# Performance work log

Hardware: AMD Instinct MI355X
Metric: run time of the kernel (lower is better)

The kernel has to match this reference:

```python
import jax, jax.numpy as jnp
import numpy as np

N = 100000
E = 2000000
F = 64          # in_features == out_features (required by attention * h_j)
BETA = 0.5
NEG_SLOPE = 0.01  # torch F.leaky_relu default


def setup_inputs() -> dict:
    key = jax.random.key(0)
    k1, k2, k3, k4, k5, k6 = jax.random.split(key, 6)
    h = jax.random.normal(k1, (N, F), dtype=jnp.float32)
    adj = jax.random.randint(k2, (2, E), 0, N, dtype=jnp.int64)
    amount = jax.random.uniform(k3, (E,), dtype=jnp.float32)
    count = jax.random.uniform(k4, (E,), dtype=jnp.float32)
    fc_w = jax.random.normal(k5, (F, 2 * F), dtype=jnp.float32) * (1.0 / np.sqrt(2 * F))
    fc_b = jax.random.normal(k6, (F,), dtype=jnp.float32) * 0.01
    return {"h": h, "adj": adj, "amount": amount, "count": count,
            "fc_w": fc_w, "fc_b": fc_b}


def _minmax_norm(x):
    lo, hi = x.min(), x.max()
    return (x - lo) / (hi - lo + 1e-8)


def reference(h, adj, amount, count, fc_w, fc_b):
    # per-edge weight from normalized amount/count
    edge_weight = BETA * _minmax_norm(amount) + (1.0 - BETA) * _minmax_norm(count)  # [E]

    src, dst = adj[0], adj[1]
    h_i = h[src]                     # [E, F]
    h_j = h[dst]                     # [E, F]
    h_cat = jnp.concatenate([h_i, h_j], axis=1)  # [E, 2F]

    score = jnp.einsum('ef,of->eo', h_cat, fc_w) + fc_b  # [E, F_out]
    score = jnp.where(score >= 0, score, NEG_SLOPE * score)  # leaky_relu
    score = score * edge_weight[:, None]

    # softmax over ALL edges (dim 0), per feature, as in the original
    attention = jax.nn.softmax(score, axis=0)  # [E, F]

    agg = jnp.zeros_like(h).at[src].add(attention * h_j)  # scatter-add -> [N, F]
    return agg
```

## Files before the change

kernel.cpp:

```cpp
#include <hip/hip_runtime.h>
#include <hip/hip_fp16.h>
#include <math.h>

#define FDIM   64
#define NB     16
#define BSHIFT 7
#define BMASK  127
#define EPTA   16
#define CHUNKA (EPTA * 256)
#define SCH    1024
#define DMASK  0xFFFFF

__global__ __launch_bounds__(256) void count_mm_k(const int* __restrict__ src,
                                                  const float* __restrict__ amount,
                                                  const float* __restrict__ count,
                                                  int* __restrict__ mat,
                                                  float4* __restrict__ partial,
                                                  double* __restrict__ colsum,
                                                  int E, int nblkA, int nbkt) {
  __shared__ int lhist[1024];
  __shared__ float4 lred[4];
  for (int k = threadIdx.x; k < nbkt; k += 256) lhist[k] = 0;
  if (blockIdx.x == 0 && threadIdx.x < 64) colsum[threadIdx.x] = 0.0;
  __syncthreads();
  float amin = 3.4e38f, amax = -3.4e38f, cmin = 3.4e38f, cmax = -3.4e38f;
  int e0 = blockIdx.x * CHUNKA + threadIdx.x * EPTA;
  if (e0 + EPTA <= E) {
    #pragma unroll
    for (int q = 0; q < EPTA; q += 4) {
      int4   s4 = *(const int4*)(src + e0 + q);
      float4 a4 = *(const float4*)(amount + e0 + q);
      float4 c4 = *(const float4*)(count + e0 + q);
      atomicAdd(&lhist[s4.x >> BSHIFT], 1);
      atomicAdd(&lhist[s4.y >> BSHIFT], 1);
      atomicAdd(&lhist[s4.z >> BSHIFT], 1);
      atomicAdd(&lhist[s4.w >> BSHIFT], 1);
      amin = fminf(amin, fminf(fminf(a4.x, a4.y), fminf(a4.z, a4.w)));
      amax = fmaxf(amax, fmaxf(fmaxf(a4.x, a4.y), fmaxf(a4.z, a4.w)));
      cmin = fminf(cmin, fminf(fminf(c4.x, c4.y), fminf(c4.z, c4.w)));
      cmax = fmaxf(cmax, fmaxf(fmaxf(c4.x, c4.y), fmaxf(c4.z, c4.w)));
    }
  } else {
    for (int e = e0; e < E; e++) {
      atomicAdd(&lhist[src[e] >> BSHIFT], 1);
      float a = amount[e], c = count[e];
      amin = fminf(amin, a); amax = fmaxf(amax, a);
      cmin = fminf(cmin, c); cmax = fmaxf(cmax, c);
    }
  }
  #pragma unroll
  for (int off = 32; off; off >>= 1) {
    amin = fminf(amin, __shfl_down(amin, off));
    amax = fmaxf(amax, __shfl_down(amax, off));
    cmin = fminf(cmin, __shfl_down(cmin, off));
    cmax = fmaxf(cmax, __shfl_down(cmax, off));
  }
  if ((threadIdx.x & 63) == 0) lred[threadIdx.x >> 6] = make_float4(amin, amax, cmin, cmax);
  __syncthreads();
  for (int k = threadIdx.x; k < nbkt; k += 256)
    mat[(size_t)k * nblkA + blockIdx.x] = lhist[k];
  if (threadIdx.x == 0) {
    float4 r = lred[0];
    #pragma unroll
    for (int w = 1; w < 4; w++) {
      r.x = fminf(r.x, lred[w].x); r.y = fmaxf(r.y, lred[w].y);
      r.z = fminf(r.z, lred[w].z); r.w = fmaxf(r.w, lred[w].w);
    }
    partial[blockIdx.x] = r;
  }
}

__global__ __launch_bounds__(256) void minmax2_k(const float4* __restrict__ partial,
                                                 float* __restrict__ mmf, int nb) {
  float amin = 3.4e38f, amax = -3.4e38f, cmin = 3.4e38f, cmax = -3.4e38f;
  for (int i = threadIdx.x; i < nb; i += 256) {
    float4 p = partial[i];
    amin = fminf(amin, p.x); amax = fmaxf(amax, p.y);
    cmin = fminf(cmin, p.z); cmax = fmaxf(cmax, p.w);
  }
  #pragma unroll
  for (int off = 32; off; off >>= 1) {
    amin = fminf(amin, __shfl_down(amin, off));
    amax = fmaxf(amax, __shfl_down(amax, off));
    cmin = fminf(cmin, __shfl_down(cmin, off));
    cmax = fmaxf(cmax, __shfl_down(cmax, off));
  }
  __shared__ float4 lds[4];
  if ((threadIdx.x & 63) == 0) lds[threadIdx.x >> 6] = make_float4(amin, amax, cmin, cmax);
  __syncthreads();
  if (threadIdx.x == 0) {
    float4 r = lds[0];
    #pragma unroll
    for (int w = 1; w < 4; w++) {
      r.x = fminf(r.x, lds[w].x); r.y = fmaxf(r.y, lds[w].y);
      r.z = fminf(r.z, lds[w].z); r.w = fmaxf(r.w, lds[w].w);
    }
    mmf[0] = r.x; mmf[1] = r.y; mmf[2] = r.z; mmf[3] = r.w;
  }
}

__global__ __launch_bounds__(256) void scan1_k(const int* __restrict__ v,
                                               int* __restrict__ bsum, int M) {
  __shared__ int lds[256];
  int t = threadIdx.x, b = blockIdx.x;
  int s = 0;
  for (int i = b * SCH + t; i < min((b + 1) * SCH, M); i += 256) s += v[i];
  lds[t] = s; __syncthreads();
  for (int off = 128; off; off >>= 1) {
    if (t < off) lds[t] += lds[t + off];
    __syncthreads();
  }
  if (t == 0) bsum[b] = lds[0];
}

__global__ __launch_bounds__(256) void scan2_k(const int* __restrict__ bsum,
                                               int* __restrict__ bexcl, int nchunk) {
  __shared__ int lds[256];
  int t = threadIdx.x;
  int running = 0;
  for (int c0 = 0; c0 < nchunk; c0 += 256) {
    int x = (c0 + t < nchunk) ? bsum[c0 + t] : 0;
    lds[t] = x; __syncthreads();
    for (int off = 1; off < 256; off <<= 1) {
      int v = (t >= off) ? lds[t - off] : 0;
      __syncthreads();
      lds[t] += v; __syncthreads();
    }
    if (c0 + t < nchunk) bexcl[c0 + t] = running + lds[t] - x;
    running += lds[255];
    __syncthreads();
  }
}

__global__ __launch_bounds__(256) void scan3_k(const int* __restrict__ v,
                                               const int* __restrict__ bexcl,
                                               int* __restrict__ smat, int M) {
  __shared__ int lds[256];
  int t = threadIdx.x, b = blockIdx.x;
  int running = bexcl[b];
  for (int tile = 0; tile < SCH; tile += 256) {
    int i = b * SCH + tile + t;
    int x = (i < M) ? v[i] : 0;
    lds[t] = x; __syncthreads();
    for (int off = 1; off < 256; off <<= 1) {
      int vv = (t >= off) ? lds[t - off] : 0;
      __syncthreads();
      lds[t] += vv; __syncthreads();
    }
    if (i < M) smat[i] = running + lds[t] - x;
    running += lds[255];
    __syncthreads();
  }
}

__global__ __launch_bounds__(256) void scatter_k(const int* __restrict__ src,
                                                 const int* __restrict__ dst,
                                                 const float* __restrict__ amount,
                                                 const float* __restrict__ count,
                                                 const float* __restrict__ mmf,
                                                 const int* __restrict__ smat,
                                                 int2* __restrict__ payload,
                                                 int E, int nblkA, int nbkt) {
  __shared__ int cntb[1024];
  __shared__ int baseb[1024];
  __shared__ int sbase[1024];
  __shared__ int tmp[256];
  __shared__ int2 lpay[CHUNKA];
  __shared__ int lgpos[CHUNKA];
  const int t = threadIdx.x, blk = blockIdx.x;
  for (int k = t; k < nbkt; k += 256) {
    cntb[k] = 0;
    sbase[k] = smat[(size_t)k * nblkA + blk];
  }
  __syncthreads();
  const float amin = mmf[0], amax = mmf[1], cmin = mmf[2], cmax = mmf[3];
  const float ascale = 0.5f / (amax - amin + 1e-8f);
  const float cscale = 0.5f / (cmax - cmin + 1e-8f);
  int e0 = blk * CHUNKA + t * EPTA;
  const bool full = (e0 + EPTA <= E);
  int4   S[4]; int4 D[4]; float4 A[4]; float4 C[4];
  if (full) {
    #pragma unroll
    for (int q = 0; q < 4; q++) {
      S[q] = *(const int4*)(src + e0 + 4 * q);
      D[q] = *(const int4*)(dst + e0 + 4 * q);
      A[q] = *(const float4*)(amount + e0 + 4 * q);
      C[q] = *(const float4*)(count + e0 + 4 * q);
      atomicAdd(&cntb[S[q].x >> BSHIFT], 1);
      atomicAdd(&cntb[S[q].y >> BSHIFT], 1);
      atomicAdd(&cntb[S[q].z >> BSHIFT], 1);
      atomicAdd(&cntb[S[q].w >> BSHIFT], 1);
    }
  } else {
    for (int e = e0; e < E; e++) atomicAdd(&cntb[src[e] >> BSHIFT], 1);
  }
  __syncthreads();
  int running = 0;
  for (int c0 = 0; c0 < nbkt; c0 += 256) {
    int x = (c0 + t < nbkt) ? cntb[c0 + t] : 0;
    tmp[t] = x; __syncthreads();
    for (int off = 1; off < 256; off <<= 1) {
      int v = (t >= off) ? tmp[t - off] : 0;
      __syncthreads();
      tmp[t] += v; __syncthreads();
    }
    if (c0 + t < nbkt) baseb[c0 + t] = running + tmp[t] - x;
    running += tmp[255];
    __syncthreads();
  }
  for (int k = t; k < nbkt; k += 256) cntb[k] = baseb[k];
  __syncthreads();
  auto ins = [&](int s, int d, float a, float c) {
    int b = s >> BSHIFT;
    float ew = (a - amin) * ascale + (c - cmin) * cscale;
    int pos = atomicAdd(&cntb[b], 1);
    lpay[pos] = make_int2(d | ((s & BMASK) << 20), __float_as_int(ew));
    lgpos[pos] = sbase[b] + (pos - baseb[b]);
  };
  if (full) {
    #pragma unroll
    for (int q = 0; q < 4; q++) {
      ins(S[q].x, D[q].x, A[q].x, C[q].x);
      ins(S[q].y, D[q].y, A[q].y, C[q].y);
      ins(S[q].z, D[q].z, A[q].z, C[q].z);
      ins(S[q].w, D[q].w, A[q].w, C[q].w);
    }
  } else {
    for (int e = e0; e < E; e++) ins(src[e], dst[e], amount[e], count[e]);
  }
  __syncthreads();
  const int ned = min(CHUNKA, E - blk * CHUNKA);
  for (int i = t; i < ned; i += 256) payload[lgpos[i]] = lpay[i];
}

__global__ __launch_bounds__(256) void binB_k(const int2* __restrict__ payload,
                                              const int* __restrict__ smat,
                                              int* __restrict__ hist,
                                              int* __restrict__ offsets,
                                              int2* __restrict__ edge_s,
                                              int E, int nblkA, int nbkt, int N) {
  __shared__ int fcnt[128];
  __shared__ int fs[128];
  __shared__ int fcur[128];
  const int b = blockIdx.x;
  const int t = threadIdx.x;
  const int base = smat[(size_t)b * nblkA];
  const int end  = (b + 1 < nbkt) ? smat[(size_t)(b + 1) * nblkA] : E;
  if (t < 128) fcnt[t] = 0;
  __syncthreads();
  for (int i = base + t; i < end; i += 256)
    atomicAdd(&fcnt[payload[i].x >> 20], 1);
  __syncthreads();
  if (t < 128) fs[t] = fcnt[t];
  __syncthreads();
  for (int off = 1; off < 128; off <<= 1) {
    int v = 0;
    if (t < 128 && t >= off) v = fs[t - off];
    __syncthreads();
    if (t < 128) fs[t] += v;
    __syncthreads();
  }
  if (t < 128) {
    int excl = fs[t] - fcnt[t];
    fcur[t] = base + excl;
    int node = (b << BSHIFT) + t;
    if (node < N) { hist[node] = fcnt[t]; offsets[node] = base + excl; }
  }
  __syncthreads();
  for (int i = base + t; i < end; i += 256) {
    int2 v = payload[i];
    int pos = atomicAdd(&fcur[v.x >> 20], 1);
    edge_s[pos] = make_int2(v.x & DMASK, v.y);
  }
}

__global__ __launch_bounds__(128) void pre_gemm(const float* __restrict__ h,
                                                const float* __restrict__ fc_w,
                                                const float* __restrict__ fc_b,
                                                float* __restrict__ G1,
                                                __half2* __restrict__ P, int N) {
  __shared__ float hs[NB * FDIM];
  const int t = threadIdx.x;
  const int o = t & 63, half = t >> 6;
  float w[FDIM];
  const float* wrow = fc_w + o * 128 + half * 64;
  #pragma unroll
  for (int f = 0; f < FDIM; f += 4) {
    float4 v = *(const float4*)(wrow + f);
    w[f] = v.x; w[f + 1] = v.y; w[f + 2] = v.z; w[f + 3] = v.w;
  }
  const float bias = (half == 0) ? fc_b[o] : 0.0f;
  const int n0 = blockIdx.x * NB;
  const int nrows = min(NB, N - n0);
  for (int i = t; i < nrows * FDIM; i += 128) hs[i] = h[(size_t)n0 * FDIM + i];
  __syncthreads();
  for (int n = 0; n < nrows; n++) {
    float acc = bias;
    #pragma unroll
    for (int f = 0; f < FDIM; f += 4) {
      float4 hv = *(const float4*)(&hs[n * FDIM + f]);
      acc += hv.x * w[f] + hv.y * w[f + 1] + hv.z * w[f + 2] + hv.w * w[f + 3];
    }
    if (half == 0) {
      G1[(size_t)(n0 + n) * FDIM + o] = acc;
    } else {
      P[(size_t)(n0 + n) * FDIM + o] =
          __halves2half2(__float2half(acc), __float2half(hs[n * FDIM + o]));
    }
  }
}

__device__ __forceinline__ float2 unpack_h2(unsigned u) {
  __half2 v = *(__half2*)&u;
  return make_float2(__low2float(v), __high2float(v));
}

__global__ __launch_bounds__(256) void fused_k(const int* __restrict__ offsets,
                                               const int* __restrict__ hist,
                                               const int2* __restrict__ edge_s,
                                               const float* __restrict__ G1,
                                               const unsigned* __restrict__ P,
                                               double* __restrict__ colsum,
                                               float* __restrict__ out, int N) {
  const int lane = threadIdx.x & 63;
  const int wid = blockIdx.x * 4 + (threadIdx.x >> 6);
  const int nw = gridDim.x * 4;
  float csum = 0.0f;
  int n = wid;
  int start = 0, cnt = 0;
  int2 p0 = make_int2(0, 0);
  float g1 = 0.0f;
  if (n < N) {
    start = offsets[n]; cnt = hist[n];
    g1 = G1[(size_t)n * FDIM + lane];
    if (lane < cnt) p0 = edge_s[start + lane];
  }
  while (n < N) {
    int nn = n + nw;
    int startN = 0, cntN = 0; float g1N = 0.0f;
    if (nn < N) {
      startN = offsets[nn]; cntN = hist[nn];
      g1N = G1[(size_t)nn * FDIM + lane];
    }
    float acc = 0.0f;
    for (int j0 = 0; j0 < cnt; j0 += 64) {
      int m = min(64, cnt - j0);
      int2 p;
      if (j0 == 0) p = p0;
      else { p = make_int2(0, 0); if (lane < m) p = edge_s[start + j0 + lane]; }
      for (int j = 0; j < m; j += 8) {
        int rem = m - j;
        int dd[8]; float ee[8], wm[8]; unsigned uu[8];
        #pragma unroll
        for (int k = 0; k < 8; k++) {
          dd[k] = __builtin_amdgcn_readlane(p.x, j + k);
          ee[k] = __int_as_float(__builtin_amdgcn_readlane(p.y, j + k));
          wm[k] = (k < rem) ? 1.0f : 0.0f;
        }
        #pragma unroll
        for (int k = 0; k < 8; k++) uu[k] = P[(size_t)dd[k] * FDIM + lane];
        #pragma unroll
        for (int k = 0; k < 8; k++) {
          float2 v = unpack_h2(uu[k]);
          float sc = g1 + v.x;
          sc = (sc >= 0.0f) ? sc : 0.01f * sc;
          float x = __expf(sc * ee[k]) * wm[k];
          csum += x;
          acc += x * v.y;
        }
      }
    }
    out[(size_t)n * FDIM + lane] = acc;
    n = nn; start = startN; cnt = cntN; g1 = g1N;
    p0 = make_int2(0, 0);
    if (n < N && lane < min(cnt, 64)) p0 = edge_s[start + lane];
  }
  __shared__ float part[256];
  part[threadIdx.x] = csum;
  __syncthreads();
  if (threadIdx.x < 64) {
    float tot = part[threadIdx.x] + part[threadIdx.x + 64] +
                part[threadIdx.x + 128] + part[threadIdx.x + 192];
    atomicAdd(&colsum[threadIdx.x], (double)tot);
  }
}

__global__ __launch_bounds__(256) void scale_k(float4* __restrict__ out4,
                                               const double* __restrict__ colsum,
                                               int total4) {
  __shared__ float rinv_s[64];
  if (threadIdx.x < 64) rinv_s[threadIdx.x] = (float)(1.0 / colsum[threadIdx.x]);
  __syncthreads();
  const float4* r4 = (const float4*)rinv_s;
  int idx = blockIdx.x * blockDim.x + threadIdx.x;
  int stride = gridDim.x * blockDim.x;
  for (int i = idx; i < total4; i += stride) {
    float4 v = out4[i];
    float4 r = r4[i & 15];
    v.x *= r.x; v.y *= r.y; v.z *= r.z; v.w *= r.w;
    out4[i] = v;
  }
}

extern "C" void kernel_launch(void* const* d_in, const int* in_sizes, int n_in,
                              void* d_out, int out_size, void* d_ws, size_t ws_size,
                              hipStream_t stream) {
  const float* h      = (const float*)d_in[0];
  const int*   adj    = (const int*)d_in[1];
  const float* amount = (const float*)d_in[2];
  const float* count  = (const float*)d_in[3];
  const float* fc_w   = (const float*)d_in[4];
  const float* fc_b   = (const float*)d_in[5];
  float* out = (float*)d_out;

  const int E = in_sizes[2];
  const int N = in_sizes[0] / FDIM;
  const int* src = adj;
  const int* dst = adj + E;
  const int nbkt  = (N + BMASK) >> BSHIFT;
  const int nblkA = (E + CHUNKA - 1) / CHUNKA;
  const int M = nbkt * nblkA;
  const int nchunk = (M + SCH - 1) / SCH;

  char* ws = (char*)d_ws;
  size_t off = 0;
  auto alloc = [&](size_t bytes) { void* p = ws + off; off += (bytes + 255) & ~(size_t)255; return p; };
  float*    G1      = (float*)alloc((size_t)N * FDIM * sizeof(float));
  __half2*  P       = (__half2*)alloc((size_t)N * FDIM * sizeof(__half2));
  int2*     edge_s  = (int2*)alloc((size_t)E * sizeof(int2));
  int2*     payload = (int2*)alloc((size_t)E * sizeof(int2));
  int*      hist    = (int*)alloc((size_t)N * sizeof(int));
  int*      offsets = (int*)alloc((size_t)N * sizeof(int));
  int*      mat     = (int*)alloc((size_t)M * sizeof(int));
  int*      smat    = (int*)alloc((size_t)M * sizeof(int));
  int*      bsum    = (int*)alloc((size_t)nchunk * sizeof(int));
  int*      bexcl   = (int*)alloc((size_t)nchunk * sizeof(int));
  float4*   mmpart  = (float4*)alloc((size_t)nblkA * sizeof(float4));
  double*   colsum  = (double*)alloc(64 * sizeof(double));
  float*    mmf     = (float*)alloc(4 * sizeof(float));

  count_mm_k<<<nblkA, 256, 0, stream>>>(src, amount, count, mat, mmpart, colsum, E, nblkA, nbkt);
  minmax2_k<<<1, 256, 0, stream>>>(mmpart, mmf, nblkA);
  scan1_k<<<nchunk, 256, 0, stream>>>(mat, bsum, M);
  scan2_k<<<1, 256, 0, stream>>>(bsum, bexcl, nchunk);
  scan3_k<<<nchunk, 256, 0, stream>>>(mat, bexcl, smat, M);
  scatter_k<<<nblkA, 256, 0, stream>>>(src, dst, amount, count, mmf, smat, payload, E, nblkA, nbkt);
  binB_k<<<nbkt, 256, 0, stream>>>(payload, smat, hist, offsets, edge_s, E, nblkA, nbkt, N);
  pre_gemm<<<(N + NB - 1) / NB, 128, 0, stream>>>(h, fc_w, fc_b, G1, P, N);
  fused_k<<<4096, 256, 0, stream>>>(offsets, hist, edge_s, G1, (const unsigned*)P, colsum, out, N);
  scale_k<<<1024, 256, 0, stream>>>((float4*)out, colsum, N * FDIM / 4);
}
```

Measured before the change: 325.6 us.

## Drop per-node binning pass; aggregate bucketed edges in LDS with shared atomics

Measured after the change: 982.8 us. 202% more time.

```diff
diff --git a/kernel.cpp b/kernel.cpp
--- a/kernel.cpp
+++ b/kernel.cpp
@@ -4,12 +4,13 @@
 
 #define FDIM   64
 #define NB     16
-#define BSHIFT 7
-#define BMASK  127
-#define EPTA   16
+#define BSHIFT 6
+#define BMASK  63
+#define EPTA   8
 #define CHUNKA (EPTA * 256)
 #define SCH    1024
 #define DMASK  0xFFFFF
+#define NBKTMX 2048
 
 __global__ __launch_bounds__(256) void count_mm_k(const int* __restrict__ src,
                                                   const float* __restrict__ amount,
@@ -18,10 +19,11 @@
                                                   float4* __restrict__ partial,
                                                   double* __restrict__ colsum,
                                                   int E, int nblkA, int nbkt) {
-  __shared__ int lhist[1024];
+  __shared__ int lhist[NBKTMX];
   __shared__ float4 lred[4];
   for (int k = threadIdx.x; k < nbkt; k += 256) lhist[k] = 0;
-  if (blockIdx.x == 0 && threadIdx.x < 64) colsum[threadIdx.x] = 0.0;
+  if (blockIdx.x == 0)
+    for (int i = threadIdx.x; i < 1024; i += 256) colsum[i] = 0.0;
   __syncthreads();
   float amin = 3.4e38f, amax = -3.4e38f, cmin = 3.4e38f, cmax = -3.4e38f;
   int e0 = blockIdx.x * CHUNKA + threadIdx.x * EPTA;
@@ -70,35 +72,6 @@
   }
 }
 
-__global__ __launch_bounds__(256) void minmax2_k(const float4* __restrict__ partial,
-                                                 float* __restrict__ mmf, int nb) {
-  float amin = 3.4e38f, amax = -3.4e38f, cmin = 3.4e38f, cmax = -3.4e38f;
-  for (int i = threadIdx.x; i < nb; i += 256) {
-    float4 p = partial[i];
-    amin = fminf(amin, p.x); amax = fmaxf(amax, p.y);
-    cmin = fminf(cmin, p.z); cmax = fmaxf(cmax, p.w);
-  }
-  #pragma unroll
-  for (int off = 32; off; off >>= 1) {
-    amin = fminf(amin, __shfl_down(amin, off));
-    amax = fmaxf(amax, __shfl_down(amax, off));
-    cmin = fminf(cmin, __shfl_down(cmin, off));
-    cmax = fmaxf(cmax, __shfl_down(cmax, off));
-  }
-  __shared__ float4 lds[4];
-  if ((threadIdx.x & 63) == 0) lds[threadIdx.x >> 6] = make_float4(amin, amax, cmin, cmax);
-  __syncthreads();
-  if (threadIdx.x == 0) {
-    float4 r = lds[0];
-    #pragma unroll
-    for (int w = 1; w < 4; w++) {
-      r.x = fminf(r.x, lds[w].x); r.y = fmaxf(r.y, lds[w].y);
-      r.z = fminf(r.z, lds[w].z); r.w = fmaxf(r.w, lds[w].w);
-    }
-    mmf[0] = r.x; mmf[1] = r.y; mmf[2] = r.z; mmf[3] = r.w;
-  }
-}
-
 __global__ __launch_bounds__(256) void scan1_k(const int* __restrict__ v,
                                                int* __restrict__ bsum, int M) {
   __shared__ int lds[256];
@@ -114,7 +87,9 @@
 }
 
 __global__ __launch_bounds__(256) void scan2_k(const int* __restrict__ bsum,
-                                               int* __restrict__ bexcl, int nchunk) {
+                                               int* __restrict__ bexcl, int nchunk,
+                                               const float4* __restrict__ partial,
+                                               float* __restrict__ mmf, int nb) {
   __shared__ int lds[256];
   int t = threadIdx.x;
   int running = 0;
@@ -129,6 +104,31 @@
     if (c0 + t < nchunk) bexcl[c0 + t] = running + lds[t] - x;
     running += lds[255];
     __syncthreads();
+  }
+  float amin = 3.4e38f, amax = -3.4e38f, cmin = 3.4e38f, cmax = -3.4e38f;
+  for (int i = t; i < nb; i += 256) {
+    float4 p = partial[i];
+    amin = fminf(amin, p.x); amax = fmaxf(amax, p.y);
+    cmin = fminf(cmin, p.z); cmax = fmaxf(cmax, p.w);
+  }
+  #pragma unroll
+  for (int off = 32; off; off >>= 1) {
+    amin = fminf(amin, __shfl_down(amin, off));
+    amax = fmaxf(amax, __shfl_down(amax, off));
+    cmin = fminf(cmin, __shfl_down(cmin, off));
+    cmax = fmaxf(cmax, __shfl_down(cmax, off));
+  }
+  __shared__ float4 lred[4];
+  if ((t & 63) == 0) lred[t >> 6] = make_float4(amin, amax, cmin, cmax);
+  __syncthreads();
+  if (t == 0) {
+    float4 r = lred[0];
+    #pragma unroll
+    for (int w = 1; w < 4; w++) {
+      r.x = fminf(r.x, lred[w].x); r.y = fmaxf(r.y, lred[w].y);
+      r.z = fminf(r.z, lred[w].z); r.w = fmaxf(r.w, lred[w].w);
+    }
+    mmf[0] = r.x; mmf[1] = r.y; mmf[2] = r.z; mmf[3] = r.w;
   }
 }
 
@@ -161,9 +161,9 @@
                                                  const int* __restrict__ smat,
                                                  int2* __restrict__ payload,
                                                  int E, int nblkA, int nbkt) {
-  __shared__ int cntb[1024];
-  __shared__ int baseb[1024];
-  __shared__ int sbase[1024];
+  __shared__ int cntb[NBKTMX];
+  __shared__ int baseb[NBKTMX];
+  __shared__ int sbase[NBKTMX];
   __shared__ int tmp[256];
   __shared__ int2 lpay[CHUNKA];
   __shared__ int lgpos[CHUNKA];
@@ -174,14 +174,15 @@
   }
   __syncthreads();
   const float amin = mmf[0], amax = mmf[1], cmin = mmf[2], cmax = mmf[3];
-  const float ascale = 0.5f / (amax - amin + 1e-8f);
-  const float cscale = 0.5f / (cmax - cmin + 1e-8f);
+  const float L2E = 1.4426950408889634f;
+  const float ascale = 0.5f * L2E / (amax - amin + 1e-8f);
+  const float cscale = 0.5f * L2E / (cmax - cmin + 1e-8f);
   int e0 = blk * CHUNKA + t * EPTA;
   const bool full = (e0 + EPTA <= E);
-  int4   S[4]; int4 D[4]; float4 A[4]; float4 C[4];
+  int4 S[EPTA / 4]; int4 D[EPTA / 4]; float4 A[EPTA / 4]; float4 C[EPTA / 4];
   if (full) {
     #pragma unroll
-    for (int q = 0; q < 4; q++) {
+    for (int q = 0; q < EPTA / 4; q++) {
       S[q] = *(const int4*)(src + e0 + 4 * q);
       D[q] = *(const int4*)(dst + e0 + 4 * q);
       A[q] = *(const float4*)(amount + e0 + 4 * q);
@@ -219,7 +220,7 @@
   };
   if (full) {
     #pragma unroll
-    for (int q = 0; q < 4; q++) {
+    for (int q = 0; q < EPTA / 4; q++) {
       ins(S[q].x, D[q].x, A[q].x, C[q].x);
       ins(S[q].y, D[q].y, A[q].y, C[q].y);
       ins(S[q].z, D[q].z, A[q].z, C[q].z);
@@ -231,47 +232,6 @@
   __syncthreads();
   const int ned = min(CHUNKA, E - blk * CHUNKA);
   for (int i = t; i < ned; i += 256) payload[lgpos[i]] = lpay[i];
-}
-
-__global__ __launch_bounds__(256) void binB_k(const int2* __restrict__ payload,
-                                              const int* __restrict__ smat,
-                                              int* __restrict__ hist,
-                                              int* __restrict__ offsets,
-                                              int2* __restrict__ edge_s,
-                                              int E, int nblkA, int nbkt, int N) {
-  __shared__ int fcnt[128];
-  __shared__ int fs[128];
-  __shared__ int fcur[128];
-  const int b = blockIdx.x;
-  const int t = threadIdx.x;
-  const int base = smat[(size_t)b * nblkA];
-  const int end  = (b + 1 < nbkt) ? smat[(size_t)(b + 1) * nblkA] : E;
-  if (t < 128) fcnt[t] = 0;
-  __syncthreads();
-  for (int i = base + t; i < end; i += 256)
-    atomicAdd(&fcnt[payload[i].x >> 20], 1);
-  __syncthreads();
-  if (t < 128) fs[t] = fcnt[t];
-  __syncthreads();
-  for (int off = 1; off < 128; off <<= 1) {
-    int v = 0;
-    if (t < 128 && t >= off) v = fs[t - off];
-    __syncthreads();
-    if (t < 128) fs[t] += v;
-    __syncthreads();
-  }
-  if (t < 128) {
-    int excl = fs[t] - fcnt[t];
-    fcur[t] = base + excl;
-    int node = (b << BSHIFT) + t;
-    if (node < N) { hist[node] = fcnt[t]; offsets[node] = base + excl; }
-  }
-  __syncthreads();
-  for (int i = base + t; i < end; i += 256) {
-    int2 v = payload[i];
-    int pos = atomicAdd(&fcur[v.x >> 20], 1);
-    edge_s[pos] = make_int2(v.x & DMASK, v.y);
-  }
 }
 
 __global__ __launch_bounds__(128) void pre_gemm(const float* __restrict__ h,
@@ -315,73 +275,90 @@
   return make_float2(__low2float(v), __high2float(v));
 }
 
-__global__ __launch_bounds__(256) void fused_k(const int* __restrict__ offsets,
-                                               const int* __restrict__ hist,
-                                               const int2* __restrict__ edge_s,
+__global__ __launch_bounds__(256) void fused_k(const int2* __restrict__ payload,
+                                               const int* __restrict__ smat,
                                                const float* __restrict__ G1,
                                                const unsigned* __restrict__ P,
                                                double* __restrict__ colsum,
-                                               float* __restrict__ out, int N) {
-  const int lane = threadIdx.x & 63;
-  const int wid = blockIdx.x * 4 + (threadIdx.x >> 6);
-  const int nw = gridDim.x * 4;
+                                               float* __restrict__ out,
+                                               int E, int nblkA, int nbkt, int N) {
+  __shared__ float g1s[64 * FDIM];
+  __shared__ float accum[64 * FDIM];
+  __shared__ float part[256];
+  const int t = threadIdx.x;
+  const int lane = t & 63;
+  const int wv = t >> 6;
+  const int b = blockIdx.x;
+  const int base = smat[(size_t)b * nblkA];
+  const int end  = (b + 1 < nbkt) ? smat[(size_t)(b + 1) * nblkA] : E;
+  const int n0 = b << BSHIFT;
+  const int nmax = min(64, N - n0);
+  {
+    const float4* Gsrc = (const float4*)(G1 + (size_t)n0 * FDIM);
+    float4* g4 = (float4*)g1s;
+    float4* a4 = (float4*)accum;
+    const int tot4 = (nmax * FDIM) >> 2;
+    for (int i = t; i < tot4; i += 256) g4[i] = Gsrc[i];
+    const float4 z = make_float4(0.f, 0.f, 0.f, 0.f);
+    for (int i = t; i < 64 * FDIM / 4; i += 256) a4[i] = z;
+  }
+  __syncthreads();
   float csum = 0.0f;
-  int n = wid;
-  int start = 0, cnt = 0;
-  int2 p0 = make_int2(0, 0);
-  float g1 = 0.0f;
-  if (n < N) {
-    start = offsets[n]; cnt = hist[n];
-    g1 = G1[(size_t)n * FDIM + lane];
-    if (lane < cnt) p0 = edge_s[start + lane];
-  }
-  while (n < N) {
-    int nn = n + nw;
-    int startN = 0, cntN = 0; float g1N = 0.0f;
-    if (nn < N) {
-      startN = offsets[nn]; cntN = hist[nn];
-      g1N = G1[(size_t)nn * FDIM + lane];
-    }
-    float acc = 0.0f;
-    for (int j0 = 0; j0 < cnt; j0 += 64) {
-      int m = min(64, cnt - j0);
-      int2 p;
-      if (j0 == 0) p = p0;
-      else { p = make_int2(0, 0); if (lane < m) p = edge_s[start + j0 + lane]; }
-      for (int j = 0; j < m; j += 8) {
-        int rem = m - j;
-        int dd[8]; float ee[8], wm[8]; unsigned uu[8];
+  for (int i0 = base + wv * 64; i0 < end; i0 += 256) {
+    const int m = min(64, end - i0);
+    int2 p = make_int2(0, 0);
+    if (lane < m) p = payload[i0 + lane];
+    if (m == 64) {
+      #pragma unroll 1
+      for (int j = 0; j < 64; j += 8) {
         #pragma unroll
         for (int k = 0; k < 8; k++) {
-          dd[k] = __builtin_amdgcn_readlane(p.x, j + k);
-          ee[k] = __int_as_float(__builtin_amdgcn_readlane(p.y, j + k));
-          wm[k] = (k < rem) ? 1.0f : 0.0f;
+          int sx = __builtin_amdgcn_readlane(p.x, j + k);
+          float ew = __int_as_float(__builtin_amdgcn_readlane(p.y, j + k));
+          int f = sx >> 20;
+          int d = sx & DMASK;
+          float g1 = g1s[f * FDIM + lane];
+          float2 v = unpack_h2(P[(size_t)d * FDIM + lane]);
+          float sc = g1 + v.x;
+          sc = fmaxf(sc, 0.01f * sc);
+          float x = exp2f(sc * ew);
+          csum += x;
+          atomicAdd(&accum[f * FDIM + lane], x * v.y);
         }
-        #pragma unroll
-        for (int k = 0; k < 8; k++) uu[k] = P[(size_t)dd[k] * FDIM + lane];
+      }
+    } else {
+      for (int j = 0; j < m; j += 8) {
+        const int rem = m - j;
         #pragma unroll
         for (int k = 0; k < 8; k++) {
-          float2 v = unpack_h2(uu[k]);
+          int sx = __builtin_amdgcn_readlane(p.x, j + k);
+          float ew = __int_as_float(__builtin_amdgcn_readlane(p.y, j + k));
+          float wm = (k < rem) ? 1.0f : 0.0f;
+          int f = sx >> 20;
+          int d = sx & DMASK;
+          float g1 = g1s[f * FDIM + lane];
+          float2 v = unpack_h2(P[(size_t)d * FDIM + lane]);
           float sc = g1 + v.x;
-          sc = (sc >= 0.0f) ? sc : 0.01f * sc;
-          float x = __expf(sc * ee[k]) * wm[k];
+          sc = fmaxf(sc, 0.01f * sc);
+          float x = exp2f(sc * ew) * wm;
           csum += x;
-          acc += x * v.y;
+          atomicAdd(&accum[f * FDIM + lane], x * v.y);
         }
       }
     }
-    out[(size_t)n * FDIM + lane] = acc;
-    n = nn; start = startN; cnt = cntN; g1 = g1N;
-    p0 = make_int2(0, 0);
-    if (n < N && lane < min(cnt, 64)) p0 = edge_s[start + lane];
-  }
-  __shared__ float part[256];
-  part[threadIdx.x] = csum;
-  __syncthreads();
-  if (threadIdx.x < 64) {
-    float tot = part[threadIdx.x] + part[threadIdx.x + 64] +
-                part[threadIdx.x + 128] + part[threadIdx.x + 192];
-    atomicAdd(&colsum[threadIdx.x], (double)tot);
+  }
+  __syncthreads();
+  {
+    float4* osrc = (float4*)(out + (size_t)n0 * FDIM);
+    const float4* a4 = (const float4*)accum;
+    const int tot4 = (nmax * FDIM) >> 2;
+    for (int i = t; i < tot4; i += 256) osrc[i] = a4[i];
+  }
+  part[t] = csum;
+  __syncthreads();
+  if (t < 64) {
+    float tot = part[t] + part[t + 64] + part[t + 128] + part[t + 192];
+    atomicAdd(&colsum[t * 16], (double)tot);
   }
 }
 
@@ -389,7 +366,7 @@
                                                const double* __restrict__ colsum,
                                                int total4) {
   __shared__ float rinv_s[64];
-  if (threadIdx.x < 64) rinv_s[threadIdx.x] = (float)(1.0 / colsum[threadIdx.x]);
+  if (threadIdx.x < 64) rinv_s[threadIdx.x] = (float)(1.0 / colsum[threadIdx.x * 16]);
   __syncthreads();
   const float4* r4 = (const float4*)rinv_s;
   int idx = blockIdx.x * blockDim.x + threadIdx.x;
@@ -427,26 +404,21 @@
   auto alloc = [&](size_t bytes) { void* p = ws + off; off += (bytes + 255) & ~(size_t)255; return p; };
   float*    G1      = (float*)alloc((size_t)N * FDIM * sizeof(float));
   __half2*  P       = (__half2*)alloc((size_t)N * FDIM * sizeof(__half2));
-  int2*     edge_s  = (int2*)alloc((size_t)E * sizeof(int2));
   int2*     payload = (int2*)alloc((size_t)E * sizeof(int2));
-  int*      hist    = (int*)alloc((size_t)N * sizeof(int));
-  int*      offsets = (int*)alloc((size_t)N * sizeof(int));
   int*      mat     = (int*)alloc((size_t)M * sizeof(int));
   int*      smat    = (int*)alloc((size_t)M * sizeof(int));
   int*      bsum    = (int*)alloc((size_t)nchunk * sizeof(int));
   int*      bexcl   = (int*)alloc((size_t)nchunk * sizeof(int));
   float4*   mmpart  = (float4*)alloc((size_t)nblkA * sizeof(float4));
-  double*   colsum  = (double*)alloc(64 * sizeof(double));
+  double*   colsum  = (double*)alloc(1024 * sizeof(double));
   float*    mmf     = (float*)alloc(4 * sizeof(float));
 
   count_mm_k<<<nblkA, 256, 0, stream>>>(src, amount, count, mat, mmpart, colsum, E, nblkA, nbkt);
-  minmax2_k<<<1, 256, 0, stream>>>(mmpart, mmf, nblkA);
   scan1_k<<<nchunk, 256, 0, stream>>>(mat, bsum, M);
-  scan2_k<<<1, 256, 0, stream>>>(bsum, bexcl, nchunk);
+  scan2_k<<<1, 256, 0, stream>>>(bsum, bexcl, nchunk, mmpart, mmf, nblkA);
   scan3_k<<<nchunk, 256, 0, stream>>>(mat, bexcl, smat, M);
   scatter_k<<<nblkA, 256, 0, stream>>>(src, dst, amount, count, mmf, smat, payload, E, nblkA, nbkt);
-  binB_k<<<nbkt, 256, 0, stream>>>(payload, smat, hist, offsets, edge_s, E, nblkA, nbkt, N);
   pre_gemm<<<(N + NB - 1) / NB, 128, 0, stream>>>(h, fc_w, fc_b, G1, P, N);
-  fused_k<<<4096, 256, 0, stream>>>(offsets, hist, edge_s, G1, (const unsigned*)P, colsum, out, N);
+  fused_k<<<nbkt, 256, 0, stream>>>(payload, smat, G1, (const unsigned*)P, colsum, out, E, nblkA, nbkt, N);
   scale_k<<<1024, 256, 0, stream>>>((float4*)out, colsum, N * FDIM / 4);
 }
```
